# Kernel optimization log

Measured on AMD Instinct MI355X. Metric: run time of the kernel, lower is better.

The kernel has to match this reference:

```python
import jax, jax.numpy as jnp
import numpy as np

B, T, S, H = 4, 128, 512, 512
LN_EPS = 1e-5


def setup_inputs() -> dict:
    key = jax.random.key(0)
    ks = jax.random.split(key, 10)
    query = jax.random.normal(ks[0], (B, T, H), dtype=jnp.float32)
    encoder_outputs = jax.random.normal(ks[1], (B, S, H), dtype=jnp.float32)
    src_lengths = jax.random.randint(ks[2], (B,), 1, S + 1, dtype=jnp.int32)
    # Parameters (nn.Linear stores weight as (out, in); we apply x @ W.T)
    W_h = jax.random.normal(ks[3], (H, H), dtype=jnp.float32) / np.sqrt(H)
    W_s = jax.random.normal(ks[4], (H, H), dtype=jnp.float32) / np.sqrt(H)
    v = jax.random.normal(ks[5], (H,), dtype=jnp.float32) * 0.01
    W_out = jax.random.normal(ks[6], (H, 2 * H), dtype=jnp.float32) / np.sqrt(2 * H)
    b_out = jnp.zeros((H,), dtype=jnp.float32)
    gamma = jnp.ones((H,), dtype=jnp.float32)
    beta = jnp.zeros((H,), dtype=jnp.float32)
    return {
        "query": query, "encoder_outputs": encoder_outputs, "src_lengths": src_lengths,
        "W_h": W_h, "W_s": W_s, "v": v, "W_out": W_out, "b_out": b_out,
        "gamma": gamma, "beta": beta,
    }


def reference(query, encoder_outputs, src_lengths, W_h, W_s, v, W_out, b_out, gamma, beta):
    # Project query and encoder states: (b,t,h) and (b,s,h)
    q_proj = jnp.einsum('bth,oh->bto', query, W_s)
    k_proj = jnp.einsum('bsh,oh->bso', encoder_outputs, W_h)
    # Additive score: tanh over broadcast-add, then dot with v -> (b,t,s)
    score = jnp.einsum('btsh,h->bts', jnp.tanh(q_proj[:, :, None, :] + k_proj[:, None, :, :]), v)
    # Mask padded source positions (src_idx >= length)
    pad = jnp.arange(S)[None, :] >= src_lengths[:, None]          # (b,s)
    score = jnp.where(pad[:, None, :], -jnp.inf, score)
    attn = jax.nn.softmax(score, axis=-1)                          # (b,t,s)
    context = jnp.einsum('bts,bsh->bth', attn, encoder_outputs)    # (b,t,h)
    cq = jnp.concatenate([context, query], axis=-1)                # (b,t,2h)
    out = jnp.tanh(jnp.einsum('btk,ok->bto', cq, W_out) + b_out)
    # LayerNorm over last dim
    mu = jnp.mean(out, axis=-1, keepdims=True)
    var = jnp.mean(jnp.square(out - mu), axis=-1, keepdims=True)
    return (out - mu) / jnp.sqrt(var + LN_EPS) * gamma + beta
```

## Files before the change

kernel.cpp:

```cpp
#include <hip/hip_runtime.h>
#include <hip/hip_bf16.h>
#include <math.h>

#define B 4
#define T 128
#define S 512
#define H 512
#define QK_SCALE 2.8853900817779268f

#if defined(__has_builtin)
#if __has_builtin(__builtin_amdgcn_exp2f)
#define EXP2F(x) __builtin_amdgcn_exp2f(x)
#else
#define EXP2F(x) __expf((x) * 0.6931471805599453f)
#endif
#else
#define EXP2F(x) __expf((x) * 0.6931471805599453f)
#endif

typedef __attribute__((ext_vector_type(8))) short bf16x8;
typedef __attribute__((ext_vector_type(4))) float f32x4;

__device__ __forceinline__ short f2b(float x) {
    unsigned int u = __float_as_uint(x);
    u += 0x7fffu + ((u >> 16) & 1u);
    return (short)(u >> 16);
}
__device__ __forceinline__ float fast_tanh(float x) {
    float e = __expf(2.0f * x);
    float r = __builtin_amdgcn_rcpf(e + 1.0f);
    return 1.0f - 2.0f * r;
}

__global__ __launch_bounds__(256) void cvt_all(
    const float* __restrict__ q, const float* __restrict__ Ws,
    const float* __restrict__ Wh, const float* __restrict__ Wo,
    const float* __restrict__ enc,
    short* __restrict__ qb, short* __restrict__ wsb, short* __restrict__ whb,
    short* __restrict__ wob, short* __restrict__ eb) {
    size_t i = ((size_t)blockIdx.x * 256 + threadIdx.x) * 8;
    const float* src; short* dst; size_t off;
    if (i < 262144)        { src = q;   dst = qb;  off = i; }
    else if (i < 524288)   { src = Ws;  dst = wsb; off = i - 262144; }
    else if (i < 786432)   { src = Wh;  dst = whb; off = i - 524288; }
    else if (i < 1310720)  { src = Wo;  dst = wob; off = i - 786432; }
    else                   { src = enc; dst = eb;  off = i - 1310720; }
    float4 a = *(const float4*)(src + off);
    float4 b = *(const float4*)(src + off + 4);
    ushort4 o0 = make_ushort4((unsigned short)f2b(a.x), (unsigned short)f2b(a.y),
                              (unsigned short)f2b(a.z), (unsigned short)f2b(a.w));
    ushort4 o1 = make_ushort4((unsigned short)f2b(b.x), (unsigned short)f2b(b.y),
                              (unsigned short)f2b(b.z), (unsigned short)f2b(b.w));
    *(ushort4*)(dst + off) = o0;
    *(ushort4*)(dst + off + 4) = o1;
}

__global__ __launch_bounds__(64) void proj_mega(
    const short* __restrict__ qb, const short* __restrict__ eb,
    const short* __restrict__ wsb, const short* __restrict__ whb,
    const short* __restrict__ wob, const int* __restrict__ slen,
    float* __restrict__ qe, float* __restrict__ ke,
    short* __restrict__ ewt, float* __restrict__ qw) {
    const int job = blockIdx.x;
    const int lane = threadIdx.x;
    const int r = lane & 15, kb = lane >> 4;
    const short* A; int lda;
    const short* W; int ldw;
    int epi;
    float* Cf = nullptr; short* Cb = nullptr; int ldc;
    if (job < 256) {
        const int m0 = (job >> 4) * 32, n0 = (job & 15) * 32;
        A = qb + (size_t)m0 * H; lda = H;
        W = wsb + (size_t)n0 * H; ldw = H;
        Cf = qe + (size_t)m0 * H + n0; ldc = H; epi = 0;
    } else if (job < 1280) {
        const int j = job - 256;
        const int m0 = (j >> 4) * 32, n0 = (j & 15) * 32;
        if ((m0 & 511) >= slen[m0 >> 9]) return;
        A = eb + (size_t)m0 * H; lda = H;
        W = whb + (size_t)n0 * H; ldw = H;
        Cf = ke + (size_t)m0 * H + n0; ldc = H; epi = 0;
    } else if (job < 2304) {
        const int j = job - 1280;
        const int b = j >> 8;
        const int m0 = ((j >> 4) & 15) * 32;
        const int n0 = (j & 15) * 32;
        if (n0 >= slen[b]) return;
        A = wob + (size_t)m0 * (2 * H); lda = 2 * H;
        W = eb + ((size_t)b * S + n0) * H; ldw = H;
        Cb = ewt + (size_t)b * H * S + (size_t)m0 * S + n0; ldc = S; epi = 1;
    } else {
        const int j = job - 2304;
        const int m0 = (j >> 4) * 32, n0 = (j & 15) * 32;
        A = qb + (size_t)m0 * H; lda = H;
        W = wob + (size_t)n0 * (2 * H) + H; ldw = 2 * H;
        Cf = qw + (size_t)m0 * H + n0; ldc = H; epi = 2;
    }
    const short* a0p = A + (size_t)r * lda + kb * 8;
    const short* a1p = a0p + (size_t)16 * lda;
    const short* b0p = W + (size_t)r * ldw + kb * 8;
    const short* b1p = b0p + (size_t)16 * ldw;
    f32x4 acc00 = {0,0,0,0}, acc01 = {0,0,0,0}, acc10 = {0,0,0,0}, acc11 = {0,0,0,0};
#pragma unroll 4
    for (int k = 0; k < H; k += 32) {
        bf16x8 a0 = *(const bf16x8*)(a0p + k);
        bf16x8 a1 = *(const bf16x8*)(a1p + k);
        bf16x8 b0 = *(const bf16x8*)(b0p + k);
        bf16x8 b1 = *(const bf16x8*)(b1p + k);
        acc00 = __builtin_amdgcn_mfma_f32_16x16x32_bf16(a0, b0, acc00, 0, 0, 0);
        acc01 = __builtin_amdgcn_mfma_f32_16x16x32_bf16(a0, b1, acc01, 0, 0, 0);
        acc10 = __builtin_amdgcn_mfma_f32_16x16x32_bf16(a1, b0, acc10, 0, 0, 0);
        acc11 = __builtin_amdgcn_mfma_f32_16x16x32_bf16(a1, b1, acc11, 0, 0, 0);
    }
    const int cr = kb * 4, cc = r;
    if (epi == 0) {
#pragma unroll
        for (int g = 0; g < 4; ++g) {
            Cf[(size_t)(cr + g) * ldc + cc]           = EXP2F(acc00[g] * QK_SCALE);
            Cf[(size_t)(cr + g) * ldc + 16 + cc]      = EXP2F(acc01[g] * QK_SCALE);
            Cf[(size_t)(16 + cr + g) * ldc + cc]      = EXP2F(acc10[g] * QK_SCALE);
            Cf[(size_t)(16 + cr + g) * ldc + 16 + cc] = EXP2F(acc11[g] * QK_SCALE);
        }
    } else if (epi == 1) {
#pragma unroll
        for (int g = 0; g < 4; ++g) {
            Cb[(size_t)(cr + g) * ldc + cc]           = f2b(acc00[g]);
            Cb[(size_t)(cr + g) * ldc + 16 + cc]      = f2b(acc01[g]);
            Cb[(size_t)(16 + cr + g) * ldc + cc]      = f2b(acc10[g]);
            Cb[(size_t)(16 + cr + g) * ldc + 16 + cc] = f2b(acc11[g]);
        }
    } else {
#pragma unroll
        for (int g = 0; g < 4; ++g) {
            Cf[(size_t)(cr + g) * ldc + cc]           = acc00[g];
            Cf[(size_t)(cr + g) * ldc + 16 + cc]      = acc01[g];
            Cf[(size_t)(16 + cr + g) * ldc + cc]      = acc10[g];
            Cf[(size_t)(16 + cr + g) * ldc + 16 + cc] = acc11[g];
        }
    }
}

__global__ __launch_bounds__(64) void score_v4(
    const float* __restrict__ qe, const float* __restrict__ ke,
    const float* __restrict__ v, const int* __restrict__ slen,
    float* __restrict__ scoreh) {
    const int qt = blockIdx.z & 3;
    const int b = blockIdx.z >> 2;
    const int L = slen[b];
    const int sbase = blockIdx.x * 16;
    if (sbase >= L) return;
    const int tbase = blockIdx.y * 8;
    const int hbase = qt * 128;
    __shared__ __align__(16) float qs[8][132];
    __shared__ __align__(16) float ks[16][132];
    __shared__ __align__(16) float vsh[128];
    const int lane = threadIdx.x;
    {
        const int r = lane >> 3, c = (lane & 7) * 16;
        const float* qsrc = qe + (size_t)(b * T + tbase + r) * H + hbase + c;
        const float* k0src = ke + (size_t)(b * S + sbase + r) * H + hbase + c;
        const float* k1src = k0src + 8 * H;
#pragma unroll
        for (int j = 0; j < 4; ++j) {
            *(float4*)&qs[r][c + j * 4] = *(const float4*)(qsrc + j * 4);
            *(float4*)&ks[r][c + j * 4] = *(const float4*)(k0src + j * 4);
            *(float4*)&ks[8 + r][c + j * 4] = *(const float4*)(k1src + j * 4);
        }
        float2 vv = *(const float2*)&v[hbase + lane * 2];
        *(float2*)&vsh[lane * 2] = make_float2(-2.f * vv.x, -2.f * vv.y);
    }
    __syncthreads();
    const int t = lane >> 3, s0 = (lane & 7) * 2;
    const float* qrow = &qs[t][0];
    const float* k0r = &ks[s0][0];
    const float* k1r = &ks[s0 + 1][0];
    float a0 = 0.f, a1 = 0.f, c0 = 0.f, c1 = 0.f;
#pragma unroll 2
    for (int i = 0; i < 128; i += 4) {
        float4 q4 = *(const float4*)&qrow[i];
        float4 ka = *(const float4*)&k0r[i];
        float4 kb = *(const float4*)&k1r[i];
        float4 v4 = *(const float4*)&vsh[i];
        a0 = fmaf(v4.x, __builtin_amdgcn_rcpf(fmaf(q4.x, ka.x, 1.f)), a0);
        c0 = fmaf(v4.x, __builtin_amdgcn_rcpf(fmaf(q4.x, kb.x, 1.f)), c0);
        a1 = fmaf(v4.y, __builtin_amdgcn_rcpf(fmaf(q4.y, ka.y, 1.f)), a1);
        c1 = fmaf(v4.y, __builtin_amdgcn_rcpf(fmaf(q4.y, kb.y, 1.f)), c1);
        a0 = fmaf(v4.z, __builtin_amdgcn_rcpf(fmaf(q4.z, ka.z, 1.f)), a0);
        c0 = fmaf(v4.z, __builtin_amdgcn_rcpf(fmaf(q4.z, kb.z, 1.f)), c0);
        a1 = fmaf(v4.w, __builtin_amdgcn_rcpf(fmaf(q4.w, ka.w, 1.f)), a1);
        c1 = fmaf(v4.w, __builtin_amdgcn_rcpf(fmaf(q4.w, kb.w, 1.f)), c1);
    }
    *(float2*)&scoreh[((size_t)qt * (B * T) + b * T + tbase + t) * S + sbase + s0] =
        make_float2(a0 + a1, c0 + c1);
}

__global__ __launch_bounds__(256) void combine_k(
    const float* __restrict__ scoreh, const int* __restrict__ slen,
    short* __restrict__ U, float* __restrict__ Z) {
    const int row = blockIdx.x * 4 + (threadIdx.x >> 6);
    const int lane = threadIdx.x & 63;
    const int L = slen[row >> 7];
    const size_t sl = (size_t)(B * T) * S;
    const float* p = scoreh + (size_t)row * S + lane * 8;
    float e[8];
    float sm = 0.f;
#pragma unroll
    for (int j = 0; j < 2; ++j) {
        float4 q0 = *(const float4*)(p + j * 4);
        float4 q1 = *(const float4*)(p + sl + j * 4);
        float4 q2 = *(const float4*)(p + 2 * sl + j * 4);
        float4 q3 = *(const float4*)(p + 3 * sl + j * 4);
        e[j * 4 + 0] = __expf(q0.x + q1.x + q2.x + q3.x);
        e[j * 4 + 1] = __expf(q0.y + q1.y + q2.y + q3.y);
        e[j * 4 + 2] = __expf(q0.z + q1.z + q2.z + q3.z);
        e[j * 4 + 3] = __expf(q0.w + q1.w + q2.w + q3.w);
    }
    const int cbase = lane * 8;
#pragma unroll
    for (int j = 0; j < 8; ++j) {
        if (cbase + j >= L) e[j] = 0.f;
        sm += e[j];
    }
#pragma unroll
    for (int off = 1; off < 64; off <<= 1) sm += __shfl_xor(sm, off);
    if (lane == 0) Z[row] = sm;
    short* o = U + (size_t)row * S + cbase;
    ushort4 u0 = make_ushort4((unsigned short)f2b(e[0]), (unsigned short)f2b(e[1]),
                              (unsigned short)f2b(e[2]), (unsigned short)f2b(e[3]));
    ushort4 u1 = make_ushort4((unsigned short)f2b(e[4]), (unsigned short)f2b(e[5]),
                              (unsigned short)f2b(e[6]), (unsigned short)f2b(e[7]));
    *(ushort4*)o = u0;
    *(ushort4*)(o + 4) = u1;
}

__global__ __launch_bounds__(64) void mfma_out2(
    const short* __restrict__ U, const short* __restrict__ ewt,
    const float* __restrict__ qw, const float* __restrict__ Z,
    const int* __restrict__ slen, const float* __restrict__ bias,
    float* __restrict__ pre) {
    const int lane = threadIdx.x;
    const int r = lane & 15, kb = lane >> 4;
    const int m0 = blockIdx.y * 32;
    const int n0 = blockIdx.x * 32;
    const int b = m0 >> 7;
    const int L = slen[b];
    const int Keff = min(S, (L + 31) & ~31);
    const short* A = U + (size_t)m0 * S;
    const short* Bp = ewt + (size_t)b * H * S;
    const short* a0p = A + (size_t)r * S + kb * 8;
    const short* a1p = a0p + 16 * S;
    const short* b0p = Bp + (size_t)(n0 + r) * S + kb * 8;
    const short* b1p = b0p + 16 * S;
    f32x4 acc00 = {0,0,0,0}, acc01 = {0,0,0,0}, acc10 = {0,0,0,0}, acc11 = {0,0,0,0};
#pragma unroll 2
    for (int k = 0; k < Keff; k += 32) {
        bf16x8 a0 = *(const bf16x8*)(a0p + k);
        bf16x8 a1 = *(const bf16x8*)(a1p + k);
        bf16x8 b0 = *(const bf16x8*)(b0p + k);
        bf16x8 b1 = *(const bf16x8*)(b1p + k);
        acc00 = __builtin_amdgcn_mfma_f32_16x16x32_bf16(a0, b0, acc00, 0, 0, 0);
        acc01 = __builtin_amdgcn_mfma_f32_16x16x32_bf16(a0, b1, acc01, 0, 0, 0);
        acc10 = __builtin_amdgcn_mfma_f32_16x16x32_bf16(a1, b0, acc10, 0, 0, 0);
        acc11 = __builtin_amdgcn_mfma_f32_16x16x32_bf16(a1, b1, acc11, 0, 0, 0);
    }
    const int cr = kb * 4, cc = r;
    float bn0 = bias[n0 + cc], bn1 = bias[n0 + 16 + cc];
#pragma unroll
    for (int g = 0; g < 4; ++g) {
        const int gr0 = m0 + cr + g;
        const int gr1 = gr0 + 16;
        float iz0 = __builtin_amdgcn_rcpf(Z[gr0]);
        float iz1 = __builtin_amdgcn_rcpf(Z[gr1]);
        size_t row0 = (size_t)gr0 * H;
        size_t row1 = (size_t)gr1 * H;
        pre[row0 + n0 + cc]      = fast_tanh(fmaf(acc00[g], iz0, qw[row0 + n0 + cc]) + bn0);
        pre[row0 + n0 + 16 + cc] = fast_tanh(fmaf(acc01[g], iz0, qw[row0 + n0 + 16 + cc]) + bn1);
        pre[row1 + n0 + cc]      = fast_tanh(fmaf(acc10[g], iz1, qw[row1 + n0 + cc]) + bn0);
        pre[row1 + n0 + 16 + cc] = fast_tanh(fmaf(acc11[g], iz1, qw[row1 + n0 + 16 + cc]) + bn1);
    }
}

__global__ __launch_bounds__(256) void ln_out(
    const float* __restrict__ X, const float* __restrict__ gamma,
    const float* __restrict__ beta, float* __restrict__ out) {
    __shared__ float red[8];
    const int r = blockIdx.x;
    const int tid = threadIdx.x;
    const int lane = tid & 63, wv = tid >> 6;
    const float* x = X + (size_t)r * H;
    float x0 = x[tid], x1 = x[tid + 256];
    float s = x0 + x1;
#pragma unroll
    for (int off = 32; off > 0; off >>= 1) s += __shfl_down(s, off);
    if (lane == 0) red[wv] = s;
    __syncthreads();
    float mu = (red[0] + red[1] + red[2] + red[3]) * (1.0f / H);
    float d0 = x0 - mu, d1 = x1 - mu;
    float vsum = d0 * d0 + d1 * d1;
#pragma unroll
    for (int off = 32; off > 0; off >>= 1) vsum += __shfl_down(vsum, off);
    if (lane == 0) red[4 + wv] = vsum;
    __syncthreads();
    float var = (red[4] + red[5] + red[6] + red[7]) * (1.0f / H);
    float inv = rsqrtf(var + 1e-5f);
    out[(size_t)r * H + tid] = d0 * inv * gamma[tid] + beta[tid];
    out[(size_t)r * H + tid + 256] = d1 * inv * gamma[tid + 256] + beta[tid + 256];
}

extern "C" void kernel_launch(void* const* d_in, const int* in_sizes, int n_in,
                              void* d_out, int out_size, void* d_ws, size_t ws_size,
                              hipStream_t stream) {
    const float* query = (const float*)d_in[0];
    const float* enc   = (const float*)d_in[1];
    const int*   slen  = (const int*)d_in[2];
    const float* W_h   = (const float*)d_in[3];
    const float* W_s   = (const float*)d_in[4];
    const float* v     = (const float*)d_in[5];
    const float* W_out = (const float*)d_in[6];
    const float* b_out = (const float*)d_in[7];
    const float* gamma = (const float*)d_in[8];
    const float* beta  = (const float*)d_in[9];
    float* out = (float*)d_out;

    char* base = (char*)d_ws;
    short* qb     = (short*)(base + 0x000000);
    short* wsb    = (short*)(base + 0x080000);
    short* whb    = (short*)(base + 0x100000);
    short* wob    = (short*)(base + 0x180000);
    short* eb     = (short*)(base + 0x280000);
    float* qe     = (float*)(base + 0x480000);
    float* ke     = (float*)(base + 0x580000);
    float* scoreh = (float*)(base + 0x980000);
    short* U      = (short*)(base + 0xD80000);
    short* ewt    = (short*)(base + 0xE00000);
    float* qw     = (float*)(base + 0x1000000);
    float* Z      = (float*)(base + 0x1100000);
    float* pre    = (float*)(base + 0x1101000);

    cvt_all<<<dim3(1152), dim3(256), 0, stream>>>(query, W_s, W_h, W_out, enc,
                                                  qb, wsb, whb, wob, eb);
    proj_mega<<<dim3(2560), dim3(64), 0, stream>>>(qb, eb, wsb, whb, wob, slen,
                                                   qe, ke, ewt, qw);
    score_v4<<<dim3(32, 16, 16), dim3(64), 0, stream>>>(qe, ke, v, slen, scoreh);
    combine_k<<<dim3(128), dim3(256), 0, stream>>>(scoreh, slen, U, Z);
    mfma_out2<<<dim3(16, 16), dim3(64), 0, stream>>>(U, ewt, qw, Z, slen, b_out, pre);
    ln_out<<<dim3(B * T), dim3(256), 0, stream>>>(pre, gamma, beta, out);
}
```

Baseline: 65.16 us.

## Retile score kernel: one source row per lane held in registers, four queries per block

Restructures the additive-score kernel so each lane owns one source position, loads its 128-wide key slice directly from global memory into registers, and computes scores against four query rows staged in shared memory. Keys no longer pass through LDS, and each thread reuses its key registers across four queries instead of sharing two keys across eight queries. Blocks now cover 64 source positions by 4 queries, so the grid changes shape and skipping of masked-out blocks becomes coarser. The trade-off is higher register use (64 floats of keys per lane) and uncoalesced per-lane row reads of keys from global memory, in exchange for fewer LDS reads per rcp.

```diff
diff --git a/kernel.cpp b/kernel.cpp
--- a/kernel.cpp
+++ b/kernel.cpp
@@ -140,58 +140,71 @@
     }
 }
 
-__global__ __launch_bounds__(64) void score_v4(
+__global__ __launch_bounds__(64) void score_v6(
     const float* __restrict__ qe, const float* __restrict__ ke,
     const float* __restrict__ v, const int* __restrict__ slen,
     float* __restrict__ scoreh) {
     const int qt = blockIdx.z & 3;
     const int b = blockIdx.z >> 2;
     const int L = slen[b];
-    const int sbase = blockIdx.x * 16;
+    const int sbase = blockIdx.x * 64;
     if (sbase >= L) return;
-    const int tbase = blockIdx.y * 8;
+    const int t0 = blockIdx.y * 4;
     const int hbase = qt * 128;
-    __shared__ __align__(16) float qs[8][132];
-    __shared__ __align__(16) float ks[16][132];
-    __shared__ __align__(16) float vsh[128];
+    __shared__ __align__(16) float qs[4][132];
+    __shared__ __align__(16) float vsh[132];
     const int lane = threadIdx.x;
     {
-        const int r = lane >> 3, c = (lane & 7) * 16;
-        const float* qsrc = qe + (size_t)(b * T + tbase + r) * H + hbase + c;
-        const float* k0src = ke + (size_t)(b * S + sbase + r) * H + hbase + c;
-        const float* k1src = k0src + 8 * H;
-#pragma unroll
-        for (int j = 0; j < 4; ++j) {
-            *(float4*)&qs[r][c + j * 4] = *(const float4*)(qsrc + j * 4);
-            *(float4*)&ks[r][c + j * 4] = *(const float4*)(k0src + j * 4);
-            *(float4*)&ks[8 + r][c + j * 4] = *(const float4*)(k1src + j * 4);
-        }
-        float2 vv = *(const float2*)&v[hbase + lane * 2];
-        *(float2*)&vsh[lane * 2] = make_float2(-2.f * vv.x, -2.f * vv.y);
+        const int tr = lane >> 4, c = (lane & 15) * 8;
+        const float* qsrc = qe + (size_t)(b * T + t0 + tr) * H + hbase + c;
+        *(float4*)&qs[tr][c]     = *(const float4*)qsrc;
+        *(float4*)&qs[tr][c + 4] = *(const float4*)(qsrc + 4);
+        if (lane < 32) {
+            float4 vv = *(const float4*)&v[hbase + lane * 4];
+            *(float4*)&vsh[lane * 4] =
+                make_float4(-2.f * vv.x, -2.f * vv.y, -2.f * vv.z, -2.f * vv.w);
+        }
     }
     __syncthreads();
-    const int t = lane >> 3, s0 = (lane & 7) * 2;
-    const float* qrow = &qs[t][0];
-    const float* k0r = &ks[s0][0];
-    const float* k1r = &ks[s0 + 1][0];
-    float a0 = 0.f, a1 = 0.f, c0 = 0.f, c1 = 0.f;
-#pragma unroll 2
-    for (int i = 0; i < 128; i += 4) {
-        float4 q4 = *(const float4*)&qrow[i];
-        float4 ka = *(const float4*)&k0r[i];
-        float4 kb = *(const float4*)&k1r[i];
-        float4 v4 = *(const float4*)&vsh[i];
-        a0 = fmaf(v4.x, __builtin_amdgcn_rcpf(fmaf(q4.x, ka.x, 1.f)), a0);
-        c0 = fmaf(v4.x, __builtin_amdgcn_rcpf(fmaf(q4.x, kb.x, 1.f)), c0);
-        a1 = fmaf(v4.y, __builtin_amdgcn_rcpf(fmaf(q4.y, ka.y, 1.f)), a1);
-        c1 = fmaf(v4.y, __builtin_amdgcn_rcpf(fmaf(q4.y, kb.y, 1.f)), c1);
-        a0 = fmaf(v4.z, __builtin_amdgcn_rcpf(fmaf(q4.z, ka.z, 1.f)), a0);
-        c0 = fmaf(v4.z, __builtin_amdgcn_rcpf(fmaf(q4.z, kb.z, 1.f)), c0);
-        a1 = fmaf(v4.w, __builtin_amdgcn_rcpf(fmaf(q4.w, ka.w, 1.f)), a1);
-        c1 = fmaf(v4.w, __builtin_amdgcn_rcpf(fmaf(q4.w, kb.w, 1.f)), c1);
-    }
-    *(float2*)&scoreh[((size_t)qt * (B * T) + b * T + tbase + t) * S + sbase + s0] =
-        make_float2(a0 + a1, c0 + c1);
+    const float* krow = ke + (size_t)(b * S + sbase + lane) * H + hbase;
+    float acc0 = 0.f, acc1 = 0.f, acc2 = 0.f, acc3 = 0.f;
+#pragma unroll
+    for (int chunk = 0; chunk < 2; ++chunk) {
+        const int ho = chunk * 64;
+        float4 kv[16];
+#pragma unroll
+        for (int j = 0; j < 16; ++j)
+            kv[j] = *(const float4*)(krow + ho + j * 4);
+#pragma unroll
+        for (int j = 0; j < 16; ++j) {
+            float4 v4 = *(const float4*)&vsh[ho + j * 4];
+            float4 q0 = *(const float4*)&qs[0][ho + j * 4];
+            float4 q1 = *(const float4*)&qs[1][ho + j * 4];
+            float4 q2 = *(const float4*)&qs[2][ho + j * 4];
+            float4 q3 = *(const float4*)&qs[3][ho + j * 4];
+            acc0 = fmaf(v4.x, __builtin_amdgcn_rcpf(fmaf(q0.x, kv[j].x, 1.f)), acc0);
+            acc1 = fmaf(v4.x, __builtin_amdgcn_rcpf(fmaf(q1.x, kv[j].x, 1.f)), acc1);
+            acc2 = fmaf(v4.x, __builtin_amdgcn_rcpf(fmaf(q2.x, kv[j].x, 1.f)), acc2);
+            acc3 = fmaf(v4.x, __builtin_amdgcn_rcpf(fmaf(q3.x, kv[j].x, 1.f)), acc3);
+            acc0 = fmaf(v4.y, __builtin_amdgcn_rcpf(fmaf(q0.y, kv[j].y, 1.f)), acc0);
+            acc1 = fmaf(v4.y, __builtin_amdgcn_rcpf(fmaf(q1.y, kv[j].y, 1.f)), acc1);
+            acc2 = fmaf(v4.y, __builtin_amdgcn_rcpf(fmaf(q2.y, kv[j].y, 1.f)), acc2);
+            acc3 = fmaf(v4.y, __builtin_amdgcn_rcpf(fmaf(q3.y, kv[j].y, 1.f)), acc3);
+            acc0 = fmaf(v4.z, __builtin_amdgcn_rcpf(fmaf(q0.z, kv[j].z, 1.f)), acc0);
+            acc1 = fmaf(v4.z, __builtin_amdgcn_rcpf(fmaf(q1.z, kv[j].z, 1.f)), acc1);
+            acc2 = fmaf(v4.z, __builtin_amdgcn_rcpf(fmaf(q2.z, kv[j].z, 1.f)), acc2);
+            acc3 = fmaf(v4.z, __builtin_amdgcn_rcpf(fmaf(q3.z, kv[j].z, 1.f)), acc3);
+            acc0 = fmaf(v4.w, __builtin_amdgcn_rcpf(fmaf(q0.w, kv[j].w, 1.f)), acc0);
+            acc1 = fmaf(v4.w, __builtin_amdgcn_rcpf(fmaf(q1.w, kv[j].w, 1.f)), acc1);
+            acc2 = fmaf(v4.w, __builtin_amdgcn_rcpf(fmaf(q2.w, kv[j].w, 1.f)), acc2);
+            acc3 = fmaf(v4.w, __builtin_amdgcn_rcpf(fmaf(q3.w, kv[j].w, 1.f)), acc3);
+        }
+    }
+    const size_t obase = ((size_t)qt * (B * T) + b * T + t0) * S + sbase + lane;
+    scoreh[obase]         = acc0;
+    scoreh[obase + S]     = acc1;
+    scoreh[obase + 2 * S] = acc2;
+    scoreh[obase + 3 * S] = acc3;
 }
 
 __global__ __launch_bounds__(256) void combine_k(
@@ -341,7 +354,7 @@
                                                   qb, wsb, whb, wob, eb);
     proj_mega<<<dim3(2560), dim3(64), 0, stream>>>(qb, eb, wsb, whb, wob, slen,
                                                    qe, ke, ewt, qw);
-    score_v4<<<dim3(32, 16, 16), dim3(64), 0, stream>>>(qe, ke, v, slen, scoreh);
+    score_v6<<<dim3(8, 32, 16), dim3(64), 0, stream>>>(qe, ke, v, slen, scoreh);
     combine_k<<<dim3(128), dim3(256), 0, stream>>>(scoreh, slen, U, Z);
     mfma_out2<<<dim3(16, 16), dim3(64), 0, stream>>>(U, ewt, qw, Z, slen, b_out, pre);
     ln_out<<<dim3(B * T), dim3(256), 0, stream>>>(pre, gamma, beta, out);
```

New measurement: 71.05 us. 9.0% more time.
